# Kernel optimization log

Measured on AMD Instinct MI355X. Metric: run time of the kernel, lower is better.

The kernel has to match this reference:

```python
import jax, jax.numpy as jnp
import numpy as np

EMBED_DIM = 2048
NUM_HEADS = 16
NUM_KV_GROUPS = 4
HEAD_DIM = EMBED_DIM // NUM_HEADS  # 128


def setup_inputs() -> dict:
    key = jax.random.key(0)
    ks = jax.random.split(key, 9)
    B, S, E = 2, 2048, EMBED_DIM
    kv_dim = HEAD_DIM * NUM_KV_GROUPS
    sc = 1.0 / np.sqrt(E)
    return {
        "x": jax.random.normal(ks[0], (B, S, E), dtype=jnp.float32),
        "Wq": jax.random.normal(ks[1], (E, E), dtype=jnp.float32) * sc,
        "bq": jnp.zeros((E,), dtype=jnp.float32),
        "Wk": jax.random.normal(ks[2], (E, kv_dim), dtype=jnp.float32) * sc,
        "bk": jnp.zeros((kv_dim,), dtype=jnp.float32),
        "Wv": jax.random.normal(ks[3], (E, kv_dim), dtype=jnp.float32) * sc,
        "bv": jnp.zeros((kv_dim,), dtype=jnp.float32),
        "Wo": jax.random.normal(ks[4], (E, E), dtype=jnp.float32) * sc,
        "bo": jnp.zeros((E,), dtype=jnp.float32),
    }


def reference(x, Wq, bq, Wk, bk, Wv, bv, Wo, bo):
    B, S, E = x.shape
    H, G, D = NUM_HEADS, NUM_KV_GROUPS, HEAD_DIM
    R = H // G  # heads per kv group
    # projections
    Q = (x @ Wq + bq).reshape(B, S, H, D).transpose(0, 2, 1, 3)   # [B,H,S,D]
    K = (x @ Wk + bk).reshape(B, S, G, D).transpose(0, 2, 1, 3)   # [B,G,S,D]
    V = (x @ Wv + bv).reshape(B, S, G, D).transpose(0, 2, 1, 3)   # [B,G,S,D]
    # GQA: broadcast KV groups over head subgroups instead of repeat_interleave copy
    Qg = Q.reshape(B, G, R, S, D)
    scores = jnp.einsum('bgrsd,bgtd->bgrst', Qg, K) / np.sqrt(D)  # [B,G,R,S,S]
    weights = jax.nn.softmax(scores, axis=-1)
    out = jnp.einsum('bgrst,bgtd->bgrsd', weights, V)             # [B,G,R,S,D]
    out = out.reshape(B, H, S, D).transpose(0, 2, 1, 3).reshape(B, S, E)
    return out @ Wo + bo
```

## Files before the change

### kernel.cpp

```cpp
#include <hip/hip_runtime.h>
#include <hip/hip_bf16.h>


typedef __attribute__((ext_vector_type(8))) short bf16x8;
typedef __attribute__((ext_vector_type(4))) short bf16x4;
typedef __attribute__((ext_vector_type(4))) float f32x4;

#define MFMA_16x16x32(a, b, c) __builtin_amdgcn_mfma_f32_16x16x32_bf16((a), (b), (c), 0, 0, 0)

__device__ __forceinline__ unsigned short f2bf(float x) {
  union { float f; unsigned int u; } c;
  c.f = x;
  unsigned int u = c.u;
  return (unsigned short)((u + 0x7fffu + ((u >> 16) & 1u)) >> 16);
}

__device__ __forceinline__ void gload_lds16(const void* g, void* l) {
  __builtin_amdgcn_global_load_lds(
      (const __attribute__((address_space(1))) unsigned int*)g,
      (__attribute__((address_space(3))) unsigned int*)l, 16, 0, 0);
}

__global__ void cast_x_kernel(const float* __restrict__ x,
                              unsigned short* __restrict__ out, long n) {
  long i = ((long)blockIdx.x * blockDim.x + threadIdx.x) * 8;
  if (i >= n) return;
  float4 a = *reinterpret_cast<const float4*>(x + i);
  float4 b = *reinterpret_cast<const float4*>(x + i + 4);
  union { unsigned short s[8]; bf16x8 v; } o;
  o.s[0] = f2bf(a.x); o.s[1] = f2bf(a.y); o.s[2] = f2bf(a.z); o.s[3] = f2bf(a.w);
  o.s[4] = f2bf(b.x); o.s[5] = f2bf(b.y); o.s[6] = f2bf(b.z); o.s[7] = f2bf(b.w);
  *reinterpret_cast<bf16x8*>(out + i) = o.v;
}

__global__ void transpose_cast_kernel(const float* __restrict__ src,
                                      unsigned short* __restrict__ dst,
                                      int K, int N) {
  __shared__ float t[32][33];
  const int tx = threadIdx.x, ty = threadIdx.y;
  const int n0 = blockIdx.x * 32, k0 = blockIdx.y * 32;
#pragma unroll
  for (int i = 0; i < 4; i++)
    t[ty + i * 8][tx] = src[(size_t)(k0 + ty + i * 8) * N + n0 + tx];
  __syncthreads();
#pragma unroll
  for (int i = 0; i < 4; i++)
    dst[(size_t)(n0 + ty + i * 8) * K + k0 + tx] = f2bf(t[tx][ty + i * 8]);
}

__global__ void concat_bias_kernel(const float* __restrict__ bq,
                                   const float* __restrict__ bk,
                                   const float* __restrict__ bv,
                                   float* __restrict__ out) {
  int i = blockIdx.x * 256 + threadIdx.x;
  if (i >= 3072) return;
  out[i] = (i < 2048) ? bq[i] : (i < 2560 ? bk[i - 2048] : bv[i - 2560]);
}

__global__ void transpose_v_kernel(const unsigned short* __restrict__ QKV,
                                   unsigned short* __restrict__ Vt) {
  __shared__ unsigned short t[32][33];
  const int tx = threadIdx.x, ty = threadIdx.y;
  const int c0 = blockIdx.x * 32;
  const int r0 = blockIdx.y * 32;
#pragma unroll
  for (int i = 0; i < 4; i++)
    t[ty + i * 8][tx] = QKV[(size_t)(r0 + ty + i * 8) * 3072 + 2560 + c0 + tx];
  __syncthreads();
#pragma unroll
  for (int i = 0; i < 4; i++) {
    const int gd = c0 + ty + i * 8;
    const int r = r0 + tx;
    const int b = r >> 11, s = r & 2047;
    const int sp = (s & ~63) | ((s & 12) << 1) | (((s >> 4) & 1) << 2) | (s & 3) | (s & 32);
    Vt[(size_t)(b * 512 + gd) * 2048 + sp] = t[tx][ty + i * 8];
  }
}

template <bool BF16OUT>
__global__ __launch_bounds__(256, 2)
void gemm_bt_kernel(const unsigned short* __restrict__ A,
                    const unsigned short* __restrict__ Bt,
                    const float* __restrict__ bias,
                    void* __restrict__ C, int M, int N, int K,
                    float qscale, int qcols) {
  __shared__ unsigned short Ash[128 * 32];
  __shared__ unsigned short Bsh[128 * 32];
  const int tid = threadIdx.x;
  const int w = tid >> 6, l = tid & 63, lg = l >> 4, ll = l & 15;
  const int wr = w >> 1, wc = w & 1;
  const int m0 = blockIdx.y * 128, n0 = blockIdx.x * 128;

  const f32x4 fz = {0.f, 0.f, 0.f, 0.f};
  f32x4 acc[4][4];
#pragma unroll
  for (int i = 0; i < 4; i++)
#pragma unroll
    for (int j = 0; j < 4; j++) acc[i][j] = fz;

  const size_t arow0 = (size_t)(m0 + (tid >> 2)) * K + (tid & 3) * 8;
  const size_t brow0 = (size_t)(n0 + (tid >> 2)) * K + (tid & 3) * 8;
  unsigned short* adst = &Ash[w * 512];
  unsigned short* bdst = &Bsh[w * 512];

  for (int k0 = 0; k0 < K; k0 += 32) {
    gload_lds16(A + arow0 + k0, adst);
    gload_lds16(A + arow0 + (size_t)64 * K + k0, adst + 2048);
    gload_lds16(Bt + brow0 + k0, bdst);
    gload_lds16(Bt + brow0 + (size_t)64 * K + k0, bdst + 2048);
    __syncthreads();
    bf16x8 af[4], bfr[4];
#pragma unroll
    for (int mi = 0; mi < 4; mi++)
      af[mi] = *reinterpret_cast<const bf16x8*>(&Ash[(wr * 64 + mi * 16 + ll) * 32 + 8 * lg]);
#pragma unroll
    for (int ni = 0; ni < 4; ni++)
      bfr[ni] = *reinterpret_cast<const bf16x8*>(&Bsh[(wc * 64 + ni * 16 + ll) * 32 + 8 * lg]);
#pragma unroll
    for (int mi = 0; mi < 4; mi++)
#pragma unroll
      for (int ni = 0; ni < 4; ni++)
        acc[mi][ni] = MFMA_16x16x32(af[mi], bfr[ni], acc[mi][ni]);
    __syncthreads();
  }

#pragma unroll
  for (int mi = 0; mi < 4; mi++) {
#pragma unroll
    for (int ni = 0; ni < 4; ni++) {
      const int gc = n0 + wc * 64 + ni * 16 + ll;
      const float bv = bias[gc];
      const float sc = (gc < qcols) ? qscale : 1.0f;
#pragma unroll
      for (int r = 0; r < 4; r++) {
        const int gr = m0 + wr * 64 + mi * 16 + 4 * lg + r;
        const float v = (acc[mi][ni][r] + bv) * sc;
        if (BF16OUT)
          ((unsigned short*)C)[(size_t)gr * N + gc] = f2bf(v);
        else
          ((float*)C)[(size_t)gr * N + gc] = v;
      }
    }
  }
}

__global__ __launch_bounds__(256, 2)
void attn_kernel(const unsigned short* __restrict__ QKV,
                 const unsigned short* __restrict__ Vt,
                 unsigned short* __restrict__ AO) {
  __shared__ unsigned short Klds[64 * 128];
  __shared__ unsigned short Vlds[128 * 64];

  const int tid = threadIdx.x;
  const int w = tid >> 6, l = tid & 63, lg = l >> 4, ll = l & 15;
  const int bh = blockIdx.y;
  const int b = bh >> 4, h = bh & 15, g = h >> 2;
  const int q0 = blockIdx.x * 128 + w * 32;
  const size_t row_base = (size_t)b * 2048 * 3072;
  const unsigned short* Vg = Vt + (size_t)(b * 512 + g * 128) * 2048;

  bf16x8 qf[2][4];
#pragma unroll
  for (int mi = 0; mi < 2; mi++)
#pragma unroll
    for (int ds = 0; ds < 4; ds++)
      qf[mi][ds] = *reinterpret_cast<const bf16x8*>(
          QKV + row_base + (size_t)(q0 + mi * 16 + ll) * 3072 + h * 128 + ds * 32 + 8 * lg);

  const f32x4 fz = {0.f, 0.f, 0.f, 0.f};
  f32x4 o[8][2];
#pragma unroll
  for (int di = 0; di < 8; di++)
#pragma unroll
    for (int mi = 0; mi < 2; mi++) o[di][mi] = fz;
  float m2[2] = {-3.0e38f, -3.0e38f}, lsum[2] = {0.f, 0.f};

  const int krow = tid >> 4, kc8 = tid & 15;
  const int vrow = tid >> 3, vc8 = tid & 7;
  const unsigned short* Kg = QKV + row_base + 2048 + g * 128 + kc8 * 8 + (size_t)krow * 3072;
  int klo[4], vlo[4];
#pragma unroll
  for (int i = 0; i < 4; i++) {
    const int kr = krow + 16 * i;
    klo[i] = (kr * 128 + kc8 * 8) ^ ((kr & 7) << 3);
    const int vr = vrow + 32 * i;
    vlo[i] = (vr * 64 + vc8 * 8) ^ ((vr & 7) << 3);
  }

  bf16x8 kreg[4], vreg[4];
#pragma unroll
  for (int i = 0; i < 4; i++) {
    kreg[i] = *reinterpret_cast<const bf16x8*>(Kg + (size_t)(16 * i) * 3072);
    vreg[i] = *reinterpret_cast<const bf16x8*>(Vg + (size_t)(vrow + 32 * i) * 2048 + vc8 * 8);
  }

  const float THR = 8.0f;

  for (int kt = 0; kt < 32; kt++) {
#pragma unroll
    for (int i = 0; i < 4; i++) *reinterpret_cast<bf16x8*>(&Klds[klo[i]]) = kreg[i];
#pragma unroll
    for (int i = 0; i < 4; i++) *reinterpret_cast<bf16x8*>(&Vlds[vlo[i]]) = vreg[i];
    __syncthreads();

    if (kt + 1 < 32) {
#pragma unroll
      for (int i = 0; i < 4; i++) {
        kreg[i] = *reinterpret_cast<const bf16x8*>(
            Kg + (size_t)((kt + 1) * 64 + 16 * i) * 3072);
        vreg[i] = *reinterpret_cast<const bf16x8*>(
            Vg + (size_t)(vrow + 32 * i) * 2048 + (kt + 1) * 64 + vc8 * 8);
      }
    }

    f32x4 st[4][2];
#pragma unroll
    for (int ni = 0; ni < 4; ni++)
#pragma unroll
      for (int mi = 0; mi < 2; mi++) st[ni][mi] = fz;
#pragma unroll
    for (int ds = 0; ds < 4; ds++) {
      bf16x8 kf[4];
#pragma unroll
      for (int ni = 0; ni < 4; ni++) {
        const int kr = ni * 16 + ll;
        kf[ni] = *reinterpret_cast<const bf16x8*>(
            &Klds[(kr * 128 + ds * 32 + 8 * lg) ^ ((kr & 7) << 3)]);
      }
#pragma unroll
      for (int ni = 0; ni < 4; ni++)
#pragma unroll
        for (int mi = 0; mi < 2; mi++)
          st[ni][mi] = MFMA_16x16x32(kf[ni], qf[mi][ds], st[ni][mi]);
    }

    float pm[2];
#pragma unroll
    for (int mi = 0; mi < 2; mi++) {
      float a0 = fmaxf(fmaxf(st[0][mi][0], st[0][mi][1]), fmaxf(st[0][mi][2], st[0][mi][3]));
      float a1 = fmaxf(fmaxf(st[1][mi][0], st[1][mi][1]), fmaxf(st[1][mi][2], st[1][mi][3]));
      float a2 = fmaxf(fmaxf(st[2][mi][0], st[2][mi][1]), fmaxf(st[2][mi][2], st[2][mi][3]));
      float a3 = fmaxf(fmaxf(st[3][mi][0], st[3][mi][1]), fmaxf(st[3][mi][2], st[3][mi][3]));
      pm[mi] = fmaxf(fmaxf(a0, a1), fmaxf(a2, a3));
      pm[mi] = fmaxf(pm[mi], __shfl_xor(pm[mi], 16, 64));
      pm[mi] = fmaxf(pm[mi], __shfl_xor(pm[mi], 32, 64));
    }
    const bool grow = (pm[0] > m2[0] + THR) || (pm[1] > m2[1] + THR);
    if (__any(grow)) {
#pragma unroll
      for (int mi = 0; mi < 2; mi++) {
        const float mn = fmaxf(m2[mi], pm[mi]);
        const float fac = __builtin_amdgcn_exp2f(m2[mi] - mn);
        m2[mi] = mn;
        lsum[mi] *= fac;
#pragma unroll
        for (int di = 0; di < 8; di++) o[di][mi] *= fac;
      }
    }
    float ps[2] = {0.f, 0.f};
#pragma unroll
    for (int ni = 0; ni < 4; ni++)
#pragma unroll
      for (int mi = 0; mi < 2; mi++)
#pragma unroll
        for (int r = 0; r < 4; r++) {
          const float pv = __builtin_amdgcn_exp2f(st[ni][mi][r] - m2[mi]);
          st[ni][mi][r] = pv;
          ps[mi] += pv;
        }
#pragma unroll
    for (int mi = 0; mi < 2; mi++) {
      ps[mi] += __shfl_xor(ps[mi], 16, 64);
      ps[mi] += __shfl_xor(ps[mi], 32, 64);
      lsum[mi] += ps[mi];
    }

    bf16x8 pf[2][2];
#pragma unroll
    for (int mi = 0; mi < 2; mi++)
#pragma unroll
      for (int ks = 0; ks < 2; ks++)
#pragma unroll
        for (int j = 0; j < 4; j++) {
          pf[mi][ks][j]     = (short)f2bf(st[2 * ks][mi][j]);
          pf[mi][ks][4 + j] = (short)f2bf(st[2 * ks + 1][mi][j]);
        }

#pragma unroll
    for (int ks = 0; ks < 2; ks++)
#pragma unroll
      for (int di = 0; di < 8; di++) {
        const int dr = di * 16 + ll;
        const bf16x8 vf = *reinterpret_cast<const bf16x8*>(
            &Vlds[(dr * 64 + ks * 32 + 8 * lg) ^ ((dr & 7) << 3)]);
#pragma unroll
        for (int mi = 0; mi < 2; mi++)
          o[di][mi] = MFMA_16x16x32(vf, pf[mi][ks], o[di][mi]);
      }
    __syncthreads();
  }

  float invl[2];
#pragma unroll
  for (int mi = 0; mi < 2; mi++) invl[mi] = 1.0f / lsum[mi];
#pragma unroll
  for (int mi = 0; mi < 2; mi++) {
    const size_t rowoff = (size_t)(b * 2048 + q0 + mi * 16 + ll) * 2048 + h * 128;
#pragma unroll
    for (int di = 0; di < 8; di++) {
      union { unsigned short s[4]; bf16x4 v; } ov;
#pragma unroll
      for (int r = 0; r < 4; r++) ov.s[r] = f2bf(o[di][mi][r] * invl[mi]);
      *reinterpret_cast<bf16x4*>(&AO[rowoff + di * 16 + 4 * lg]) = ov.v;
    }
  }
}

extern "C" void kernel_launch(void* const* d_in, const int* in_sizes, int n_in,
                              void* d_out, int out_size, void* d_ws, size_t ws_size,
                              hipStream_t stream) {
  const float* x  = (const float*)d_in[0];
  const float* Wq = (const float*)d_in[1];
  const float* bq = (const float*)d_in[2];
  const float* Wk = (const float*)d_in[3];
  const float* bk = (const float*)d_in[4];
  const float* Wv = (const float*)d_in[5];
  const float* bv = (const float*)d_in[6];
  const float* Wo = (const float*)d_in[7];
  const float* bo = (const float*)d_in[8];
  float* out = (float*)d_out;

  unsigned short* xb    = (unsigned short*)d_ws;
  unsigned short* Vt    = xb;
  unsigned short* WqkvT = xb + (size_t)4096 * 2048;
  unsigned short* WoT   = WqkvT + (size_t)3072 * 2048;
  unsigned short* QKV   = WoT + (size_t)2048 * 2048;
  unsigned short* AO    = QKV + (size_t)4096 * 3072;
  float* bqkv = (float*)(AO + (size_t)4096 * 2048);

  const float QSC2 = 0.08838834764831845f * 1.4426950408889634f;

  cast_x_kernel<<<4096, 256, 0, stream>>>(x, xb, (long)8388608);
  transpose_cast_kernel<<<dim3(64, 64), dim3(32, 8), 0, stream>>>(Wq, WqkvT, 2048, 2048);
  transpose_cast_kernel<<<dim3(16, 64), dim3(32, 8), 0, stream>>>(Wk, WqkvT + (size_t)2048 * 2048, 2048, 512);
  transpose_cast_kernel<<<dim3(16, 64), dim3(32, 8), 0, stream>>>(Wv, WqkvT + (size_t)2560 * 2048, 2048, 512);
  transpose_cast_kernel<<<dim3(64, 64), dim3(32, 8), 0, stream>>>(Wo, WoT, 2048, 2048);
  concat_bias_kernel<<<12, 256, 0, stream>>>(bq, bk, bv, bqkv);

  gemm_bt_kernel<true><<<dim3(24, 32), 256, 0, stream>>>(xb, WqkvT, bqkv, QKV, 4096, 3072, 2048, QSC2, 2048);
  transpose_v_kernel<<<dim3(16, 128), dim3(32, 8), 0, stream>>>(QKV, Vt);
  attn_kernel<<<dim3(16, 32), 256, 0, stream>>>(QKV, Vt, AO);
  gemm_bt_kernel<false><<<dim3(16, 32), 256, 0, stream>>>(AO, WoT, bo, out, 4096, 2048, 2048, 1.0f, 0);
}
```

Before: 226.2 us.

## Replace GEMM kernel with multi-buffered pipelined 512-thread larger-tile GEMM

Replaces the single-buffered 128x128 GEMM with a templated kernel that uses 512 threads, larger block tiles (256x256 for QKV, 128x256 for the output projection) and a four-slot LDS ring that is filled two k-steps ahead. Loads are waited on with explicit vmcnt counts, and MFMA sections are bracketed with setprio so global-to-LDS loads overlap compute. The aim is to hide memory latency and cut the per-k-step barriers of the old loop. In exchange the kernel uses much more LDS and more accumulator registers, which may limit occupancy, and the QKV grid shrinks to 192 blocks.

```diff
diff --git a/kernel.cpp b/kernel.cpp
--- a/kernel.cpp
+++ b/kernel.cpp
@@ -77,65 +77,109 @@
   }
 }
 
-template <bool BF16OUT>
-__global__ __launch_bounds__(256, 2)
-void gemm_bt_kernel(const unsigned short* __restrict__ A,
-                    const unsigned short* __restrict__ Bt,
-                    const float* __restrict__ bias,
-                    void* __restrict__ C, int M, int N, int K,
-                    float qscale, int qcols) {
-  __shared__ unsigned short Ash[128 * 32];
-  __shared__ unsigned short Bsh[128 * 32];
+template <int ARNDS, int BRNDS, bool BF16OUT>
+__global__ __launch_bounds__(512, 2)
+void gemm_pipe_kernel(const unsigned short* __restrict__ A,
+                      const unsigned short* __restrict__ Bt,
+                      const float* __restrict__ bias,
+                      void* __restrict__ C, int M, int N, int K,
+                      float qscale, int qcols) {
+  constexpr int FM = ARNDS * 4;
+  constexpr int FN = BRNDS * 2;
+  constexpr int HFM = FM / 2;
+  constexpr int BUFE = (ARNDS + BRNDS) * 4096;
+  __shared__ unsigned short lds[4 * BUFE];
+
   const int tid = threadIdx.x;
   const int w = tid >> 6, l = tid & 63, lg = l >> 4, ll = l & 15;
-  const int wr = w >> 1, wc = w & 1;
-  const int m0 = blockIdx.y * 128, n0 = blockIdx.x * 128;
+  const int wm = w >> 2, wn = w & 3;
+  const int m0 = blockIdx.y * (ARNDS * 128);
+  const int n0 = blockIdx.x * (BRNDS * 128);
+  const int NT = K >> 5;
 
   const f32x4 fz = {0.f, 0.f, 0.f, 0.f};
-  f32x4 acc[4][4];
-#pragma unroll
-  for (int i = 0; i < 4; i++)
-#pragma unroll
-    for (int j = 0; j < 4; j++) acc[i][j] = fz;
-
-  const size_t arow0 = (size_t)(m0 + (tid >> 2)) * K + (tid & 3) * 8;
-  const size_t brow0 = (size_t)(n0 + (tid >> 2)) * K + (tid & 3) * 8;
-  unsigned short* adst = &Ash[w * 512];
-  unsigned short* bdst = &Bsh[w * 512];
-
-  for (int k0 = 0; k0 < K; k0 += 32) {
-    gload_lds16(A + arow0 + k0, adst);
-    gload_lds16(A + arow0 + (size_t)64 * K + k0, adst + 2048);
-    gload_lds16(Bt + brow0 + k0, bdst);
-    gload_lds16(Bt + brow0 + (size_t)64 * K + k0, bdst + 2048);
-    __syncthreads();
-    bf16x8 af[4], bfr[4];
-#pragma unroll
-    for (int mi = 0; mi < 4; mi++)
-      af[mi] = *reinterpret_cast<const bf16x8*>(&Ash[(wr * 64 + mi * 16 + ll) * 32 + 8 * lg]);
-#pragma unroll
-    for (int ni = 0; ni < 4; ni++)
-      bfr[ni] = *reinterpret_cast<const bf16x8*>(&Bsh[(wc * 64 + ni * 16 + ll) * 32 + 8 * lg]);
-#pragma unroll
-    for (int mi = 0; mi < 4; mi++)
-#pragma unroll
-      for (int ni = 0; ni < 4; ni++)
-        acc[mi][ni] = MFMA_16x16x32(af[mi], bfr[ni], acc[mi][ni]);
-    __syncthreads();
-  }
-
-#pragma unroll
-  for (int mi = 0; mi < 4; mi++) {
-#pragma unroll
-    for (int ni = 0; ni < 4; ni++) {
-      const int gc = n0 + wc * 64 + ni * 16 + ll;
+  f32x4 acc[FM][FN];
+#pragma unroll
+  for (int i = 0; i < FM; i++)
+#pragma unroll
+    for (int j = 0; j < FN; j++) acc[i][j] = fz;
+
+  const int srow = tid >> 2, schunk = tid & 3;
+  const unsigned short* Ag = A + (size_t)(m0 + srow) * K + schunk * 8;
+  const unsigned short* Bg = Bt + (size_t)(n0 + srow) * K + schunk * 8;
+
+  auto stageA = [&](int t) {
+    unsigned short* dst = &lds[(t & 3) * BUFE + tid * 8];
+#pragma unroll
+    for (int r = 0; r < ARNDS; ++r)
+      gload_lds16(Ag + (size_t)(r * 128) * K + t * 32, dst + r * 4096);
+  };
+  auto stageB = [&](int t) {
+    unsigned short* dst = &lds[(t & 3) * BUFE + ARNDS * 4096 + tid * 8];
+#pragma unroll
+    for (int r = 0; r < BRNDS; ++r)
+      gload_lds16(Bg + (size_t)(r * 128) * K + t * 32, dst + r * 4096);
+  };
+
+  stageA(0); stageB(0);
+  stageA(1); stageB(1);
+
+  for (int t = 0; t < NT; ++t) {
+    if (t + 1 < NT) {
+      if constexpr (ARNDS + BRNDS == 4)
+        asm volatile("s_waitcnt vmcnt(4)" ::: "memory");
+      else
+        asm volatile("s_waitcnt vmcnt(3)" ::: "memory");
+    } else {
+      asm volatile("s_waitcnt vmcnt(0)" ::: "memory");
+    }
+    __builtin_amdgcn_s_barrier();
+    const unsigned short* bufp = &lds[(t & 3) * BUFE];
+
+    bf16x8 bfrag[FN], afrag[HFM];
+#pragma unroll
+    for (int ni = 0; ni < FN; ++ni)
+      bfrag[ni] = *reinterpret_cast<const bf16x8*>(
+          &bufp[ARNDS * 4096 + (wn * FN * 16 + ni * 16 + ll) * 32 + lg * 8]);
+#pragma unroll
+    for (int mi = 0; mi < HFM; ++mi)
+      afrag[mi] = *reinterpret_cast<const bf16x8*>(
+          &bufp[(wm * FM * 16 + mi * 16 + ll) * 32 + lg * 8]);
+    if (t + 2 < NT) stageA(t + 2);
+    __builtin_amdgcn_s_setprio(1);
+#pragma unroll
+    for (int mi = 0; mi < HFM; ++mi)
+#pragma unroll
+      for (int ni = 0; ni < FN; ++ni)
+        acc[mi][ni] = MFMA_16x16x32(afrag[mi], bfrag[ni], acc[mi][ni]);
+    __builtin_amdgcn_s_setprio(0);
+
+#pragma unroll
+    for (int mi = 0; mi < HFM; ++mi)
+      afrag[mi] = *reinterpret_cast<const bf16x8*>(
+          &bufp[(wm * FM * 16 + (HFM + mi) * 16 + ll) * 32 + lg * 8]);
+    if (t + 2 < NT) stageB(t + 2);
+    __builtin_amdgcn_s_setprio(1);
+#pragma unroll
+    for (int mi = 0; mi < HFM; ++mi)
+#pragma unroll
+      for (int ni = 0; ni < FN; ++ni)
+        acc[HFM + mi][ni] = MFMA_16x16x32(afrag[mi], bfrag[ni], acc[HFM + mi][ni]);
+    __builtin_amdgcn_s_setprio(0);
+  }
+
+#pragma unroll
+  for (int mi = 0; mi < FM; ++mi) {
+#pragma unroll
+    for (int ni = 0; ni < FN; ++ni) {
+      const int gc = n0 + wn * FN * 16 + ni * 16 + ll;
       const float bv = bias[gc];
       const float sc = (gc < qcols) ? qscale : 1.0f;
 #pragma unroll
-      for (int r = 0; r < 4; r++) {
-        const int gr = m0 + wr * 64 + mi * 16 + 4 * lg + r;
+      for (int r = 0; r < 4; ++r) {
+        const int gr = m0 + wm * FM * 16 + mi * 16 + 4 * lg + r;
         const float v = (acc[mi][ni][r] + bv) * sc;
-        if (BF16OUT)
+        if constexpr (BF16OUT)
           ((unsigned short*)C)[(size_t)gr * N + gc] = f2bf(v);
         else
           ((float*)C)[(size_t)gr * N + gc] = v;
@@ -347,8 +391,10 @@
   transpose_cast_kernel<<<dim3(64, 64), dim3(32, 8), 0, stream>>>(Wo, WoT, 2048, 2048);
   concat_bias_kernel<<<12, 256, 0, stream>>>(bq, bk, bv, bqkv);
 
-  gemm_bt_kernel<true><<<dim3(24, 32), 256, 0, stream>>>(xb, WqkvT, bqkv, QKV, 4096, 3072, 2048, QSC2, 2048);
+  gemm_pipe_kernel<2, 2, true><<<dim3(12, 16), 512, 0, stream>>>(
+      xb, WqkvT, bqkv, QKV, 4096, 3072, 2048, QSC2, 2048);
   transpose_v_kernel<<<dim3(16, 128), dim3(32, 8), 0, stream>>>(QKV, Vt);
   attn_kernel<<<dim3(16, 32), 256, 0, stream>>>(QKV, Vt, AO);
-  gemm_bt_kernel<false><<<dim3(16, 32), 256, 0, stream>>>(AO, WoT, bo, out, 4096, 2048, 2048, 1.0f, 0);
-}
+  gemm_pipe_kernel<1, 2, false><<<dim3(8, 32), 512, 0, stream>>>(
+      AO, WoT, bo, out, 4096, 2048, 2048, 1.0f, 0);
+}
```

After: 215.5 us. 4.7% less time.
